# Kernel optimization log

Hardware: AMD Instinct MI355X
Metric: run time of the kernel (lower is better)

## Reference

```python
import jax, jax.numpy as jnp
import numpy as np

B, N, C = 8, 4096, 1024
H, D = 16, 64
FF = 4096
EPS_ATTN = 1e-6
EPS_LN = 1e-5


def layer_norm(x, g, b, eps=EPS_LN):
    mu = jnp.mean(x, axis=-1, keepdims=True)
    var = jnp.mean(jnp.square(x - mu), axis=-1, keepdims=True)
    return (x - mu) * jax.lax.rsqrt(var + eps) * g + b


def phi(x):
    # elu(x) + 1
    return jnp.where(x > 0, x + 1.0, jnp.exp(x))


def setup_inputs() -> dict:
    key = jax.random.key(0)
    ks = jax.random.split(key, 8)
    src = jax.random.normal(ks[0], (B, N, C), dtype=jnp.float32)
    lengths = jax.random.randint(ks[1], (B,), int(0.75 * N), N + 1)
    src_key_padding_mask = jnp.arange(N)[None, :] >= lengths[:, None]
    s = 0.02
    qkv_w = jax.random.normal(ks[2], (3 * C, C), dtype=jnp.float32) * s
    qkv_b = jnp.zeros((3 * C,), jnp.float32)
    out_w = jax.random.normal(ks[3], (C, C), dtype=jnp.float32) * s
    out_b = jnp.zeros((C,), jnp.float32)
    w1 = jax.random.normal(ks[4], (FF, C), dtype=jnp.float32) * s
    b1 = jnp.zeros((FF,), jnp.float32)
    w2 = jax.random.normal(ks[5], (C, FF), dtype=jnp.float32) * s
    b2 = jnp.zeros((C,), jnp.float32)
    ln1_g = jnp.ones((C,), jnp.float32)
    ln1_b = jnp.zeros((C,), jnp.float32)
    ln2_g = jnp.ones((C,), jnp.float32)
    ln2_b = jnp.zeros((C,), jnp.float32)
    return dict(src=src, src_key_padding_mask=src_key_padding_mask,
                qkv_w=qkv_w, qkv_b=qkv_b, out_w=out_w, out_b=out_b,
                w1=w1, b1=b1, w2=w2, b2=b2,
                ln1_g=ln1_g, ln1_b=ln1_b, ln2_g=ln2_g, ln2_b=ln2_b)


def linear_attention(x, mask, qkv_w, qkv_b, out_w, out_b):
    b, n, c = x.shape
    qkv = (x @ qkv_w.T + qkv_b).reshape(b, n, 3, H, D)
    qkv = jnp.transpose(qkv, (2, 0, 3, 1, 4))  # [3,B,H,N,D]
    q, k, v = qkv[0], qkv[1], qkv[2]
    qf, kf = phi(q), phi(k)
    valid = (~mask).astype(kf.dtype)[:, None, :, None]  # [B,1,N,1]
    kf = kf * valid
    v = v * valid
    kv = jnp.einsum('bhnd,bhne->bhde', kf, v)          # [B,H,D,D]
    z = kf.sum(axis=2)                                  # [B,H,D]
    y_num = jnp.einsum('bhnd,bhde->bhne', qf, kv)       # [B,H,N,D]
    y_den = jnp.maximum(jnp.einsum('bhnd,bhd->bhn', qf, z), EPS_ATTN)
    y = y_num / y_den[..., None]
    y = jnp.transpose(y, (0, 2, 1, 3)).reshape(b, n, c)
    return y @ out_w.T + out_b


def reference(src, src_key_padding_mask, qkv_w, qkv_b, out_w, out_b,
              w1, b1, w2, b2, ln1_g, ln1_b, ln2_g, ln2_b):
    # pre-norm: attention block
    attn_out = linear_attention(layer_norm(src, ln1_g, ln1_b), src_key_padding_mask,
                                qkv_w, qkv_b, out_w, out_b)
    x = src + attn_out
    # pre-norm: FFN block (exact gelu, matching torch F.gelu default)
    h = jax.nn.gelu(layer_norm(x, ln2_g, ln2_b) @ w1.T + b1, approximate=False)
    return x + (h @ w2.T + b2)
```

## Files before the change

### kernel.cpp

```cpp
#include <hip/hip_runtime.h>
#include <cmath>
#include <cstdint>

#define MTOK 32768
#define CDIM 1024
#define SEQ  4096
#define NHEAD 16
#define HDIM 64
#define FFDIM 4096

typedef __attribute__((ext_vector_type(8))) short short8;
typedef __attribute__((ext_vector_type(4))) float f32x4;

static __device__ __forceinline__ float b2f(unsigned short u){
  union { unsigned int i; float f; } c; c.i = ((unsigned int)u)<<16; return c.f;
}
static __device__ __forceinline__ unsigned short f2b(float f){
  union { float f; unsigned int i; } c; c.f = f;
  return (unsigned short)((c.i + 0x7fffu + ((c.i>>16)&1u)) >> 16);
}
static __device__ __forceinline__ void nt_store_us(unsigned short v, unsigned short* p){
  __builtin_nontemporal_store(v, p);
}
static __device__ __forceinline__ void nt_store_f(float v, float* p){
  __builtin_nontemporal_store(v, p);
}
static __device__ __forceinline__ void async16(const void* g, void* l){
  __builtin_amdgcn_global_load_lds((const __attribute__((address_space(1))) void*)g,
                                   (__attribute__((address_space(3))) void*)l, 16, 0, 0);
}

__global__ void detect_mask_kernel(const unsigned int* __restrict__ m, int* __restrict__ flag){
  __shared__ int any;
  if(threadIdx.x==0) any=0;
  __syncthreads();
  int loc=0;
  for(int i=threadIdx.x;i<8192;i+=256) if(m[i]>1u) loc=1;
  if(loc) atomicOr(&any,1);
  __syncthreads();
  if(threadIdx.x==0) *flag=any;
}
__global__ void decode_mask_kernel(const void* __restrict__ m, const int* __restrict__ flag,
                                   float* __restrict__ validf){
  int i = blockIdx.x*256 + threadIdx.x;
  int pad = (*flag) ? (int)((const unsigned char*)m)[i] : ((const int*)m)[i];
  validf[i] = pad ? 0.f : 1.f;
}

__global__ void cast_all_kernel(const float* __restrict__ a, const float* __restrict__ b,
                                const float* __restrict__ c, const float* __restrict__ d,
                                unsigned short* __restrict__ oa, unsigned short* __restrict__ ob,
                                unsigned short* __restrict__ oc, unsigned short* __restrict__ od){
  long i = ((long)blockIdx.x*256 + threadIdx.x)*4;
  const float* x; unsigned short* y; long off;
  if(i < 3145728){ x=a; y=oa; off=i; }
  else if(i < 4194304){ x=b; y=ob; off=i-3145728; }
  else if(i < 8388608){ x=c; y=oc; off=i-4194304; }
  else { x=d; y=od; off=i-8388608; }
  float4 v = *(const float4*)(x+off);
  ushort4 o; o.x=f2b(v.x); o.y=f2b(v.y); o.z=f2b(v.z); o.w=f2b(v.w);
  *(ushort4*)(y+off)=o;
}

__global__ __launch_bounds__(256) void ln_kernel(const float* __restrict__ x,
    const float* __restrict__ g, const float* __restrict__ bt, unsigned short* __restrict__ out){
  int row = blockIdx.x, t = threadIdx.x;
  const float* xr = x + (size_t)row*CDIM;
  float4 v = *(const float4*)(xr + t*4);
  float s1 = v.x+v.y+v.z+v.w;
  float s2 = v.x*v.x+v.y*v.y+v.z*v.z+v.w*v.w;
  #pragma unroll
  for(int off=32; off>0; off>>=1){ s1+=__shfl_down(s1,off); s2+=__shfl_down(s2,off); }
  __shared__ float a1[4], a2[4];
  __shared__ float mu_s, rs_s;
  if((t&63)==0){ a1[t>>6]=s1; a2[t>>6]=s2; }
  __syncthreads();
  if(t==0){
    float u1=a1[0]+a1[1]+a1[2]+a1[3], u2=a2[0]+a2[1]+a2[2]+a2[3];
    float mu=u1*(1.f/CDIM);
    mu_s=mu; rs_s=rsqrtf(u2*(1.f/CDIM)-mu*mu+1e-5f);
  }
  __syncthreads();
  float mu=mu_s, rs=rs_s;
  float4 gg=*(const float4*)(g+t*4), bb=*(const float4*)(bt+t*4);
  ushort4 o;
  o.x=f2b((v.x-mu)*rs*gg.x+bb.x);
  o.y=f2b((v.y-mu)*rs*gg.y+bb.y);
  o.z=f2b((v.z-mu)*rs*gg.z+bb.z);
  o.w=f2b((v.w-mu)*rs*gg.w+bb.w);
  *(ushort4*)(out+(size_t)row*CDIM+t*4)=o;
}

template<int MODE>
__global__ __launch_bounds__(256,2) void gemm_bt(
    const unsigned short* __restrict__ A, const unsigned short* __restrict__ Bw,
    const float* __restrict__ bias, const float* __restrict__ extra,
    float* __restrict__ Cf, unsigned short* __restrict__ Cb,
    int M, int N, int K)
{
  __shared__ __align__(16) unsigned short As[128*64];
  __shared__ __align__(16) unsigned short Bs[128*64];
  const int tid = threadIdx.x;
  const int wave = tid>>6, lane = tid&63;
  const int wm = wave>>1, wn = wave&1;
  const int f   = blockIdx.y * gridDim.x + blockIdx.x;
  const int xcd = f & 7, kk = f >> 3;
  const int nx  = kk % gridDim.x;
  const int ny  = (kk / gridDim.x) * 8 + xcd;
  const int m0 = ny*128, n0 = nx*128;
  const int lrow = lane>>3;
  const int gcol = (((lane&7) ^ lrow))*8;

  f32x4 acc[4][4];
  #pragma unroll
  for(int i=0;i<4;i++)
    #pragma unroll
    for(int j=0;j<4;j++) acc[i][j]=(f32x4)(0.f);

  const int ar = wm*64 + (lane&15);
  const int br = wn*64 + (lane&15);
  const int kc = lane>>4;
  const int xorv = lane&7;

  for(int kt=0; kt<K; kt+=64){
    #pragma unroll
    for(int it=0; it<4; it++){
      int wo = wave*4+it;
      int r  = wo*8 + lrow;
      async16(A  + (size_t)(m0+r)*K + kt + gcol, (void*)&As[wo*512]);
      async16(Bw + (size_t)(n0+r)*K + kt + gcol, (void*)&Bs[wo*512]);
    }
    __syncthreads();
    #pragma unroll
    for(int ks=0; ks<2; ks++){
      const int ch = ((ks*4 + kc) ^ xorv)*8;
      short8 a[4], b[4];
      #pragma unroll
      for(int i=0;i<4;i++){
        a[i]=*(const short8*)&As[(ar+i*16)*64 + ch];
        b[i]=*(const short8*)&Bs[(br+i*16)*64 + ch];
      }
      #pragma unroll
      for(int i=0;i<4;i++)
        #pragma unroll
        for(int j=0;j<4;j++)
          acc[i][j]=__builtin_amdgcn_mfma_f32_16x16x32_bf16(a[i],b[j],acc[i][j],0,0,0);
    }
    __syncthreads();
  }
  const int rbase = m0 + wm*64 + (lane>>4)*4;
  const int cbase = n0 + wn*64 + (lane&15);
  #pragma unroll
  for(int mi=0;mi<4;mi++){
    #pragma unroll
    for(int i=0;i<4;i++){
      int m = rbase + mi*16 + i;
      #pragma unroll
      for(int ni=0;ni<4;ni++){
        int n = cbase + ni*16;
        float v = acc[mi][ni][i] + bias[n];
        if(MODE==0){
          float valid = extra[m];
          int part = n>>10;
          float p = (v>0.f)? (v+1.f) : __expf(v);
          float r = (part==0)? p : (part==1? p*valid : v*valid);
          nt_store_us(f2b(r), &Cb[(size_t)m*N + n]);
        } else if(MODE==1){
          size_t off=(size_t)m*N+n;
          Cf[off] = v + extra[off];
        } else if(MODE==2){
          float gl = 0.5f*v*(1.f+erff(v*0.70710678118654752f));
          nt_store_us(f2b(gl), &Cb[(size_t)m*N+n]);
        } else {
          size_t off=(size_t)m*N+n;
          nt_store_f(Cf[off] + v, &Cf[off]);
        }
      }
    }
  }
}

__global__ __launch_bounds__(256) void kvz_partial_kernel(
    const unsigned short* __restrict__ qkv, float* __restrict__ kvp, float* __restrict__ zp)
{
  const int chunk = blockIdx.x;
  const int bh = blockIdx.y;
  const int b = bh>>4, h = bh&15;
  const int t = threadIdx.x;
  __shared__ float kfs[64][64];
  __shared__ float vs[64][64];
  float acc[4][4]={{0}}; float zacc[4]={0};
  const int td=t&15, te=t>>4;
  const int d0=td*4, e0=te*4;
  const int lr=t>>4, lc=(t&15)*4;
  for(int s=0;s<4;s++){
    __syncthreads();
    #pragma unroll
    for(int rr=0; rr<4; rr++){
      int row = rr*16 + lr;
      size_t m  = (size_t)(b*SEQ + chunk*256 + s*64 + row);
      size_t rb = m*3072 + (size_t)h*64;
      ushort4 k4 = *(const ushort4*)(qkv + rb + 1024 + lc);
      ushort4 v4 = *(const ushort4*)(qkv + rb + 2048 + lc);
      kfs[row][lc]=b2f(k4.x); kfs[row][lc+1]=b2f(k4.y); kfs[row][lc+2]=b2f(k4.z); kfs[row][lc+3]=b2f(k4.w);
      vs [row][lc]=b2f(v4.x); vs [row][lc+1]=b2f(v4.y); vs [row][lc+2]=b2f(v4.z); vs [row][lc+3]=b2f(v4.w);
    }
    __syncthreads();
    #pragma unroll 8
    for(int n=0;n<64;n++){
      float4 kq=*(const float4*)&kfs[n][d0];
      float4 vv=*(const float4*)&vs[n][e0];
      float kqa[4]={kq.x,kq.y,kq.z,kq.w};
      float vva[4]={vv.x,vv.y,vv.z,vv.w};
      #pragma unroll
      for(int i=0;i<4;i++)
        #pragma unroll
        for(int j=0;j<4;j++) acc[i][j]+=kqa[i]*vva[j];
      if(te==0){ zacc[0]+=kq.x; zacc[1]+=kq.y; zacc[2]+=kq.z; zacc[3]+=kq.w; }
    }
  }
  const int pidx = bh*16 + chunk;
  float* kvd = kvp + (size_t)pidx*4096;
  #pragma unroll
  for(int i=0;i<4;i++){
    float4 o={acc[i][0],acc[i][1],acc[i][2],acc[i][3]};
    *(float4*)(kvd + (d0+i)*64 + e0)=o;
  }
  if(te==0){
    float4 o={zacc[0],zacc[1],zacc[2],zacc[3]};
    *(float4*)(zp + (size_t)pidx*64 + d0)=o;
  }
}

__global__ void kvz_reduce_kernel(const float* __restrict__ kvp, const float* __restrict__ zp,
                                  float* __restrict__ kv, float* __restrict__ z){
  int bh = blockIdx.x, t = threadIdx.x;
  for(int j=t; j<4096; j+=256){
    float s=0;
    for(int c=0;c<16;c++) s += kvp[((size_t)bh*16+c)*4096 + j];
    kv[(size_t)bh*4096 + j] = s;
  }
  if(t<64){
    float s=0;
    for(int c=0;c<16;c++) s += zp[((size_t)bh*16+c)*64 + t];
    z[bh*64+t]=s;
  }
}

__global__ __launch_bounds__(256) void y_kernel(
    const unsigned short* __restrict__ qkv, const float* __restrict__ kv,
    const float* __restrict__ z, unsigned short* __restrict__ ybuf)
{
  const int nch = blockIdx.x;
  const int bh  = blockIdx.y;
  const int b = bh>>4, h = bh&15;
  const int t = threadIdx.x;
  __shared__ float kvs[64][64];
  __shared__ float qfs[64][68];
  __shared__ float zs[64];
  for(int j=t*4; j<4096; j+=1024){
    float4 vv=*(const float4*)(kv+(size_t)bh*4096+j);
    ((float*)kvs)[j]=vv.x; ((float*)kvs)[j+1]=vv.y; ((float*)kvs)[j+2]=vv.z; ((float*)kvs)[j+3]=vv.w;
  }
  if(t<64) zs[t]=z[bh*64+t];
  for(int s=0;s<4;s++){
    int row=s*16+(t>>4), col=(t&15)*4;
    size_t m=(size_t)(b*SEQ+nch*64+row);
    ushort4 q4=*(const ushort4*)(qkv+m*3072+(size_t)h*64+col);
    qfs[row][col]=b2f(q4.x); qfs[row][col+1]=b2f(q4.y); qfs[row][col+2]=b2f(q4.z); qfs[row][col+3]=b2f(q4.w);
  }
  __syncthreads();
  const int tn=t>>4, te=t&15;
  const int nr0=tn*4, e0=te*4;
  float acc[4][4]={{0}}; float den[4]={0};
  #pragma unroll 4
  for(int d=0;d<64;d++){
    float4 kv4=*(const float4*)&kvs[d][e0];
    float zd=zs[d];
    #pragma unroll
    for(int i=0;i<4;i++){
      float q=qfs[nr0+i][d];
      acc[i][0]+=q*kv4.x; acc[i][1]+=q*kv4.y; acc[i][2]+=q*kv4.z; acc[i][3]+=q*kv4.w;
      den[i]+=q*zd;
    }
  }
  #pragma unroll
  for(int i=0;i<4;i++){
    float inv=1.f/fmaxf(den[i],1e-6f);
    ushort4 o;
    o.x=f2b(acc[i][0]*inv); o.y=f2b(acc[i][1]*inv); o.z=f2b(acc[i][2]*inv); o.w=f2b(acc[i][3]*inv);
    size_t m=(size_t)(b*SEQ+nch*64+nr0+i);
    *(ushort4*)(ybuf+m*1024+(size_t)h*64+e0)=o;
  }
}

extern "C" void kernel_launch(void* const* d_in, const int* in_sizes, int n_in,
                              void* d_out, int out_size, void* d_ws, size_t ws_size,
                              hipStream_t stream)
{
  const float* src   = (const float*)d_in[0];
  const void*  mask  = d_in[1];
  const float* qkv_w = (const float*)d_in[2];
  const float* qkv_b = (const float*)d_in[3];
  const float* out_w = (const float*)d_in[4];
  const float* out_b = (const float*)d_in[5];
  const float* w1    = (const float*)d_in[6];
  const float* b1    = (const float*)d_in[7];
  const float* w2    = (const float*)d_in[8];
  const float* b2    = (const float*)d_in[9];
  const float* ln1g  = (const float*)d_in[10];
  const float* ln1b  = (const float*)d_in[11];
  const float* ln2g  = (const float*)d_in[12];
  const float* ln2b  = (const float*)d_in[13];
  float* out = (float*)d_out;
  char* ws = (char*)d_ws;

  size_t o = 0;
  int* flag = (int*)(ws);                         o += 256;
  float* validf = (float*)(ws+o);                 o += (size_t)MTOK*4;
  unsigned short* wqb = (unsigned short*)(ws+o);  o += (size_t)3072*1024*2;
  unsigned short* wob = (unsigned short*)(ws+o);  o += (size_t)1024*1024*2;
  unsigned short* w1b = (unsigned short*)(ws+o);  o += (size_t)4096*1024*2;
  unsigned short* w2b = (unsigned short*)(ws+o);  o += (size_t)1024*4096*2;
  unsigned short* bufA = (unsigned short*)(ws+o); o += (size_t)MTOK*1024*2;
  char* R = ws+o;                                 o += (size_t)MTOK*4096*2;
  unsigned short* qkvbuf = (unsigned short*)R;
  float* kvp = (float*)(R + (size_t)MTOK*3072*2);
  float* zp  = (float*)(R + (size_t)MTOK*3072*2 + (size_t)2048*4096*4);
  unsigned short* hbuf = (unsigned short*)R;
  float* kv = (float*)(ws+o);                     o += (size_t)128*4096*4;
  float* zv = (float*)(ws+o);                     o += (size_t)128*64*4;

  detect_mask_kernel<<<1,256,0,stream>>>((const unsigned int*)mask, flag);
  decode_mask_kernel<<<MTOK/256,256,0,stream>>>(mask, flag, validf);
  cast_all_kernel<<<12288,256,0,stream>>>(qkv_w, out_w, w1, w2, wqb, wob, w1b, w2b);

  ln_kernel<<<MTOK,256,0,stream>>>(src, ln1g, ln1b, bufA);
  gemm_bt<0><<<dim3(3072/128, MTOK/128),256,0,stream>>>(bufA, wqb, qkv_b, validf, nullptr, qkvbuf, MTOK,3072,1024);
  kvz_partial_kernel<<<dim3(16,128),256,0,stream>>>(qkvbuf, kvp, zp);
  kvz_reduce_kernel<<<128,256,0,stream>>>(kvp, zp, kv, zv);
  y_kernel<<<dim3(64,128),256,0,stream>>>(qkvbuf, kv, zv, bufA);
  gemm_bt<1><<<dim3(1024/128, MTOK/128),256,0,stream>>>(bufA, wob, out_b, src, out, nullptr, MTOK,1024,1024);
  ln_kernel<<<MTOK,256,0,stream>>>(out, ln2g, ln2b, bufA);
  gemm_bt<2><<<dim3(4096/128, MTOK/128),256,0,stream>>>(bufA, w1b, b1, nullptr, nullptr, hbuf, MTOK,4096,1024);
  gemm_bt<3><<<dim3(1024/128, MTOK/128),256,0,stream>>>(hbuf, w2b, b2, nullptr, out, nullptr, MTOK,1024,4096);
}
```

Measured before the change: 1.467 ms.

## Move linear-attention kv and y computations onto MFMA with transposed K/V layout

The QKV GEMM epilogue now writes Q row-major and K and V transposed per head (d-major over sequence), so the kv outer product can run as a bf16 MFMA GEMM in a new single-wave kernel using 32 chunks per head. The reduce kernel packs kv transposed plus z as an extra row in bf16. The y pass becomes an MFMA GEMM whose fifth column tile computes the denominator. The GEMM tile-to-block mapping is also swizzled into 4x8 groups for better L2 reuse, and nontemporal stores are dropped. In exchange, kv and z are rounded to bf16 before multiplying with Q, which reduces precision, and the transposed K/V stores are strided.

```diff
diff --git a/kernel.cpp b/kernel.cpp
--- a/kernel.cpp
+++ b/kernel.cpp
@@ -18,12 +18,6 @@
 static __device__ __forceinline__ unsigned short f2b(float f){
   union { float f; unsigned int i; } c; c.f = f;
   return (unsigned short)((c.i + 0x7fffu + ((c.i>>16)&1u)) >> 16);
-}
-static __device__ __forceinline__ void nt_store_us(unsigned short v, unsigned short* p){
-  __builtin_nontemporal_store(v, p);
-}
-static __device__ __forceinline__ void nt_store_f(float v, float* p){
-  __builtin_nontemporal_store(v, p);
 }
 static __device__ __forceinline__ void async16(const void* g, void* l){
   __builtin_amdgcn_global_load_lds((const __attribute__((address_space(1))) void*)g,
@@ -96,6 +90,7 @@
     const unsigned short* __restrict__ A, const unsigned short* __restrict__ Bw,
     const float* __restrict__ bias, const float* __restrict__ extra,
     float* __restrict__ Cf, unsigned short* __restrict__ Cb,
+    unsigned short* __restrict__ Kt, unsigned short* __restrict__ Vt,
     int M, int N, int K)
 {
   __shared__ __align__(16) unsigned short As[128*64];
@@ -103,10 +98,15 @@
   const int tid = threadIdx.x;
   const int wave = tid>>6, lane = tid&63;
   const int wm = wave>>1, wn = wave&1;
-  const int f   = blockIdx.y * gridDim.x + blockIdx.x;
-  const int xcd = f & 7, kk = f >> 3;
-  const int nx  = kk % gridDim.x;
-  const int ny  = (kk / gridDim.x) * 8 + xcd;
+  const int gx  = gridDim.x;
+  const int f   = blockIdx.y * gx + blockIdx.x;
+  const int xcd = f & 7;
+  const int kk  = f >> 3;
+  const int idx = kk & 31, g = kk >> 5;
+  const int nq  = gx >> 2;
+  const int gxq = g % nq, gy = g / nq;
+  const int nx  = gxq*4 + (idx>>3);
+  const int ny  = (gy*8 + (idx&7))*8 + xcd;
   const int m0 = ny*128, n0 = nx*128;
   const int lrow = lane>>3;
   const int gcol = (((lane&7) ^ lrow))*8;
@@ -150,147 +150,203 @@
   }
   const int rbase = m0 + wm*64 + (lane>>4)*4;
   const int cbase = n0 + wn*64 + (lane&15);
-  #pragma unroll
-  for(int mi=0;mi<4;mi++){
-    #pragma unroll
-    for(int i=0;i<4;i++){
-      int m = rbase + mi*16 + i;
+  if(MODE==0){
+    #pragma unroll
+    for(int mi=0;mi<4;mi++){
+      int mrow = rbase + mi*16;
+      float4 vld = *(const float4*)(extra + mrow);
+      float vv[4] = {vld.x, vld.y, vld.z, vld.w};
       #pragma unroll
       for(int ni=0;ni<4;ni++){
         int n = cbase + ni*16;
-        float v = acc[mi][ni][i] + bias[n];
-        if(MODE==0){
-          float valid = extra[m];
-          int part = n>>10;
-          float p = (v>0.f)? (v+1.f) : __expf(v);
-          float r = (part==0)? p : (part==1? p*valid : v*valid);
-          nt_store_us(f2b(r), &Cb[(size_t)m*N + n]);
-        } else if(MODE==1){
-          size_t off=(size_t)m*N+n;
-          Cf[off] = v + extra[off];
-        } else if(MODE==2){
-          float gl = 0.5f*v*(1.f+erff(v*0.70710678118654752f));
-          nt_store_us(f2b(gl), &Cb[(size_t)m*N+n]);
+        float bs = bias[n];
+        int part = n>>10;
+        if(part==0){
+          #pragma unroll
+          for(int i=0;i<4;i++){
+            float v = acc[mi][ni][i] + bs;
+            float p = (v>0.f)? (v+1.f) : __expf(v);
+            Cb[(size_t)(mrow+i)*1024 + n] = f2b(p);
+          }
         } else {
-          size_t off=(size_t)m*N+n;
-          nt_store_f(Cf[off] + v, &Cf[off]);
+          int d = n & 63, hh = (n>>6) & 15;
+          int bb_ = mrow >> 12, pos = mrow & 4095;
+          unsigned short* dst = (part==1? Kt : Vt)
+              + (((size_t)(bb_*16+hh)*64 + d)*SEQ + pos);
+          ushort4 o;
+          #pragma unroll
+          for(int i=0;i<4;i++){
+            float v = acc[mi][ni][i] + bs;
+            float r = (part==1)? (((v>0.f)?(v+1.f):__expf(v))*vv[i]) : (v*vv[i]);
+            ((unsigned short*)&o)[i] = f2b(r);
+          }
+          *(ushort4*)dst = o;
         }
       }
     }
-  }
-}
-
-__global__ __launch_bounds__(256) void kvz_partial_kernel(
-    const unsigned short* __restrict__ qkv, float* __restrict__ kvp, float* __restrict__ zp)
+  } else {
+    #pragma unroll
+    for(int mi=0;mi<4;mi++){
+      #pragma unroll
+      for(int i=0;i<4;i++){
+        int m = rbase + mi*16 + i;
+        #pragma unroll
+        for(int ni=0;ni<4;ni++){
+          int n = cbase + ni*16;
+          float v = acc[mi][ni][i] + bias[n];
+          if(MODE==1){
+            size_t off=(size_t)m*N+n;
+            Cf[off] = v + extra[off];
+          } else if(MODE==2){
+            float gl = 0.5f*v*(1.f+erff(v*0.70710678118654752f));
+            Cb[(size_t)m*N+n] = f2b(gl);
+          } else {
+            size_t off=(size_t)m*N+n;
+            Cf[off] += v;
+          }
+        }
+      }
+    }
+  }
+}
+
+__global__ __launch_bounds__(64) void kvz_mfma_kernel(
+    const unsigned short* __restrict__ Kt, const unsigned short* __restrict__ Vt,
+    float* __restrict__ kvp, float* __restrict__ zp)
 {
-  const int chunk = blockIdx.x;
-  const int bh = blockIdx.y;
-  const int b = bh>>4, h = bh&15;
-  const int t = threadIdx.x;
-  __shared__ float kfs[64][64];
-  __shared__ float vs[64][64];
-  float acc[4][4]={{0}}; float zacc[4]={0};
-  const int td=t&15, te=t>>4;
-  const int d0=td*4, e0=te*4;
-  const int lr=t>>4, lc=(t&15)*4;
-  for(int s=0;s<4;s++){
-    __syncthreads();
-    #pragma unroll
-    for(int rr=0; rr<4; rr++){
-      int row = rr*16 + lr;
-      size_t m  = (size_t)(b*SEQ + chunk*256 + s*64 + row);
-      size_t rb = m*3072 + (size_t)h*64;
-      ushort4 k4 = *(const ushort4*)(qkv + rb + 1024 + lc);
-      ushort4 v4 = *(const ushort4*)(qkv + rb + 2048 + lc);
-      kfs[row][lc]=b2f(k4.x); kfs[row][lc+1]=b2f(k4.y); kfs[row][lc+2]=b2f(k4.z); kfs[row][lc+3]=b2f(k4.w);
-      vs [row][lc]=b2f(v4.x); vs [row][lc+1]=b2f(v4.y); vs [row][lc+2]=b2f(v4.z); vs [row][lc+3]=b2f(v4.w);
-    }
-    __syncthreads();
-    #pragma unroll 8
-    for(int n=0;n<64;n++){
-      float4 kq=*(const float4*)&kfs[n][d0];
-      float4 vv=*(const float4*)&vs[n][e0];
-      float kqa[4]={kq.x,kq.y,kq.z,kq.w};
-      float vva[4]={vv.x,vv.y,vv.z,vv.w};
+  __shared__ __align__(16) unsigned short Ks[2][64*64];
+  __shared__ __align__(16) unsigned short Vs[2][64*64];
+  const int blk = blockIdx.x;
+  const int bh = blk>>5, kcn = blk&31;
+  const int n0 = kcn*128;
+  const int lane = threadIdx.x;
+  const int r8 = lane>>3;
+  const int gch = ((lane&7) ^ r8)*8;
+  const size_t base = (size_t)bh*64*SEQ + n0 + gch;
+  #pragma unroll
+  for(int t=0;t<2;t++){
+    #pragma unroll
+    for(int wo=0;wo<8;wo++){
+      int r = wo*8 + r8;
+      async16(Kt + base + (size_t)r*SEQ + t*64, (void*)&Ks[t][wo*512]);
+      async16(Vt + base + (size_t)r*SEQ + t*64, (void*)&Vs[t][wo*512]);
+    }
+  }
+  asm volatile("s_waitcnt vmcnt(0)" ::: "memory");
+  f32x4 acc[4][4];
+  #pragma unroll
+  for(int i=0;i<4;i++)
+    #pragma unroll
+    for(int j=0;j<4;j++) acc[i][j]=(f32x4)(0.f);
+  float zacc[4]={0.f,0.f,0.f,0.f};
+  const int l15 = lane&15, kc4 = lane>>4, x7 = lane&7;
+  #pragma unroll
+  for(int t=0;t<2;t++){
+    #pragma unroll
+    for(int ks=0; ks<2; ks++){
+      const int ch = ((ks*4 + kc4) ^ x7)*8;
+      short8 a[4], b[4];
+      #pragma unroll
+      for(int i=0;i<4;i++) a[i]=*(const short8*)&Vs[t][(l15+i*16)*64 + ch];
+      #pragma unroll
+      for(int j=0;j<4;j++) b[j]=*(const short8*)&Ks[t][(l15+j*16)*64 + ch];
+      #pragma unroll
+      for(int j=0;j<4;j++)
+        #pragma unroll
+        for(int e8=0;e8<8;e8++) zacc[j] += b2f((unsigned short)b[j][e8]);
       #pragma unroll
       for(int i=0;i<4;i++)
         #pragma unroll
-        for(int j=0;j<4;j++) acc[i][j]+=kqa[i]*vva[j];
-      if(te==0){ zacc[0]+=kq.x; zacc[1]+=kq.y; zacc[2]+=kq.z; zacc[3]+=kq.w; }
-    }
-  }
-  const int pidx = bh*16 + chunk;
-  float* kvd = kvp + (size_t)pidx*4096;
-  #pragma unroll
-  for(int i=0;i<4;i++){
-    float4 o={acc[i][0],acc[i][1],acc[i][2],acc[i][3]};
-    *(float4*)(kvd + (d0+i)*64 + e0)=o;
-  }
-  if(te==0){
-    float4 o={zacc[0],zacc[1],zacc[2],zacc[3]};
-    *(float4*)(zp + (size_t)pidx*64 + d0)=o;
-  }
+        for(int j=0;j<4;j++)
+          acc[i][j]=__builtin_amdgcn_mfma_f32_16x16x32_bf16(a[i],b[j],acc[i][j],0,0,0);
+    }
+  }
+  #pragma unroll
+  for(int j=0;j<4;j++){
+    float v = zacc[j];
+    v += __shfl_down(v, 32);
+    v += __shfl_down(v, 16);
+    if(lane<16) zp[(size_t)blk*64 + j*16 + lane] = v;
+  }
+  float* kvd = kvp + (size_t)blk*4096;
+  #pragma unroll
+  for(int i=0;i<4;i++)
+    #pragma unroll
+    for(int j=0;j<4;j++)
+      #pragma unroll
+      for(int r=0;r<4;r++)
+        kvd[(i*16 + kc4*4 + r)*64 + j*16 + l15] = acc[i][j][r];
 }
 
 __global__ void kvz_reduce_kernel(const float* __restrict__ kvp, const float* __restrict__ zp,
-                                  float* __restrict__ kv, float* __restrict__ z){
+                                  unsigned short* __restrict__ kvtb){
   int bh = blockIdx.x, t = threadIdx.x;
-  for(int j=t; j<4096; j+=256){
-    float s=0;
-    for(int c=0;c<16;c++) s += kvp[((size_t)bh*16+c)*4096 + j];
-    kv[(size_t)bh*4096 + j] = s;
-  }
-  if(t<64){
-    float s=0;
-    for(int c=0;c<16;c++) s += zp[((size_t)bh*16+c)*64 + t];
-    z[bh*64+t]=s;
-  }
-}
-
-__global__ __launch_bounds__(256) void y_kernel(
-    const unsigned short* __restrict__ qkv, const float* __restrict__ kv,
-    const float* __restrict__ z, unsigned short* __restrict__ ybuf)
+  for(int idx=t; idx<5120; idx+=256){
+    int e = idx>>6, d = idx&63;
+    float s = 0.f;
+    if(e < 64){
+      for(int c=0;c<32;c++) s += kvp[((size_t)bh*32+c)*4096 + e*64 + d];
+    } else if(e == 64){
+      for(int c=0;c<32;c++) s += zp[((size_t)bh*32+c)*64 + d];
+    }
+    kvtb[(size_t)bh*5120 + idx] = f2b(s);
+  }
+}
+
+__global__ __launch_bounds__(256) void y_gemm_kernel(
+    const unsigned short* __restrict__ qb, const unsigned short* __restrict__ kvtb,
+    unsigned short* __restrict__ ybuf)
 {
-  const int nch = blockIdx.x;
-  const int bh  = blockIdx.y;
-  const int b = bh>>4, h = bh&15;
-  const int t = threadIdx.x;
-  __shared__ float kvs[64][64];
-  __shared__ float qfs[64][68];
-  __shared__ float zs[64];
-  for(int j=t*4; j<4096; j+=1024){
-    float4 vv=*(const float4*)(kv+(size_t)bh*4096+j);
-    ((float*)kvs)[j]=vv.x; ((float*)kvs)[j+1]=vv.y; ((float*)kvs)[j+2]=vv.z; ((float*)kvs)[j+3]=vv.w;
-  }
-  if(t<64) zs[t]=z[bh*64+t];
-  for(int s=0;s<4;s++){
-    int row=s*16+(t>>4), col=(t&15)*4;
-    size_t m=(size_t)(b*SEQ+nch*64+row);
-    ushort4 q4=*(const ushort4*)(qkv+m*3072+(size_t)h*64+col);
-    qfs[row][col]=b2f(q4.x); qfs[row][col+1]=b2f(q4.y); qfs[row][col+2]=b2f(q4.z); qfs[row][col+3]=b2f(q4.w);
+  __shared__ __align__(16) unsigned short As[128*64];
+  __shared__ __align__(16) unsigned short Bs[80*64];
+  const int tid = threadIdx.x, lane = tid&63, wave = tid>>6;
+  const int bh = blockIdx.y, b = bh>>4, h = bh&15;
+  const int m0 = blockIdx.x*128;
+  const int r8 = lane>>3, gch = ((lane&7)^r8)*8;
+  const unsigned short* qbase = qb + ((size_t)(b*SEQ + m0))*1024 + h*64 + gch;
+  #pragma unroll
+  for(int it=0; it<4; it++){
+    int wo = wave*4 + it, r = wo*8 + r8;
+    async16(qbase + (size_t)r*1024, (void*)&As[wo*512]);
+  }
+  const unsigned short* kvb = kvtb + (size_t)bh*5120 + gch;
+  #pragma unroll
+  for(int it=0; it<3; it++){
+    int wo = wave + it*4;
+    if(wo < 10){ int r = wo*8 + r8; async16(kvb + r*64, (void*)&Bs[wo*512]); }
   }
   __syncthreads();
-  const int tn=t>>4, te=t&15;
-  const int nr0=tn*4, e0=te*4;
-  float acc[4][4]={{0}}; float den[4]={0};
-  #pragma unroll 4
-  for(int d=0;d<64;d++){
-    float4 kv4=*(const float4*)&kvs[d][e0];
-    float zd=zs[d];
-    #pragma unroll
-    for(int i=0;i<4;i++){
-      float q=qfs[nr0+i][d];
-      acc[i][0]+=q*kv4.x; acc[i][1]+=q*kv4.y; acc[i][2]+=q*kv4.z; acc[i][3]+=q*kv4.w;
-      den[i]+=q*zd;
-    }
-  }
-  #pragma unroll
-  for(int i=0;i<4;i++){
-    float inv=1.f/fmaxf(den[i],1e-6f);
-    ushort4 o;
-    o.x=f2b(acc[i][0]*inv); o.y=f2b(acc[i][1]*inv); o.z=f2b(acc[i][2]*inv); o.w=f2b(acc[i][3]*inv);
-    size_t m=(size_t)(b*SEQ+nch*64+nr0+i);
-    *(ushort4*)(ybuf+m*1024+(size_t)h*64+e0)=o;
+  const int l15 = lane&15, kc4 = lane>>4, x7 = lane&7;
+  f32x4 acc[2][5];
+  #pragma unroll
+  for(int i=0;i<2;i++)
+    #pragma unroll
+    for(int j=0;j<5;j++) acc[i][j]=(f32x4)(0.f);
+  #pragma unroll
+  for(int ks=0; ks<2; ks++){
+    const int ch = ((ks*4 + kc4) ^ x7)*8;
+    short8 a[2], bb[5];
+    #pragma unroll
+    for(int i=0;i<2;i++) a[i]=*(const short8*)&As[(wave*32 + i*16 + l15)*64 + ch];
+    #pragma unroll
+    for(int j=0;j<5;j++) bb[j]=*(const short8*)&Bs[(j*16 + l15)*64 + ch];
+    #pragma unroll
+    for(int i=0;i<2;i++)
+      #pragma unroll
+      for(int j=0;j<5;j++)
+        acc[i][j]=__builtin_amdgcn_mfma_f32_16x16x32_bf16(a[i],bb[j],acc[i][j],0,0,0);
+  }
+  #pragma unroll
+  for(int i=0;i<2;i++){
+    #pragma unroll
+    for(int r=0;r<4;r++){
+      float den = __shfl(acc[i][4][r], lane & 48);
+      float inv = 1.f/fmaxf(den, 1e-6f);
+      size_t m = (size_t)(b*SEQ + m0 + wave*32 + i*16 + kc4*4 + r);
+      #pragma unroll
+      for(int j=0;j<4;j++)
+        ybuf[m*1024 + h*64 + j*16 + l15] = f2b(acc[i][j][r]*inv);
+    }
   }
 }
 
@@ -324,24 +380,28 @@
   unsigned short* w2b = (unsigned short*)(ws+o);  o += (size_t)1024*4096*2;
   unsigned short* bufA = (unsigned short*)(ws+o); o += (size_t)MTOK*1024*2;
   char* R = ws+o;                                 o += (size_t)MTOK*4096*2;
-  unsigned short* qkvbuf = (unsigned short*)R;
+  unsigned short* qb  = (unsigned short*)R;
+  unsigned short* ktb = (unsigned short*)(R + (size_t)MTOK*1024*2);
+  unsigned short* vtb = (unsigned short*)(R + (size_t)MTOK*2048*2);
   float* kvp = (float*)(R + (size_t)MTOK*3072*2);
-  float* zp  = (float*)(R + (size_t)MTOK*3072*2 + (size_t)2048*4096*4);
   unsigned short* hbuf = (unsigned short*)R;
   float* kv = (float*)(ws+o);                     o += (size_t)128*4096*4;
   float* zv = (float*)(ws+o);                     o += (size_t)128*64*4;
+  float* zp = (float*)(ws+o);                     o += (size_t)4096*64*4;
+  unsigned short* kvtb = (unsigned short*)(ws+o); o += (size_t)128*5120*2;
+  (void)kv; (void)zv;
 
   detect_mask_kernel<<<1,256,0,stream>>>((const unsigned int*)mask, flag);
   decode_mask_kernel<<<MTOK/256,256,0,stream>>>(mask, flag, validf);
   cast_all_kernel<<<12288,256,0,stream>>>(qkv_w, out_w, w1, w2, wqb, wob, w1b, w2b);
 
   ln_kernel<<<MTOK,256,0,stream>>>(src, ln1g, ln1b, bufA);
-  gemm_bt<0><<<dim3(3072/128, MTOK/128),256,0,stream>>>(bufA, wqb, qkv_b, validf, nullptr, qkvbuf, MTOK,3072,1024);
-  kvz_partial_kernel<<<dim3(16,128),256,0,stream>>>(qkvbuf, kvp, zp);
-  kvz_reduce_kernel<<<128,256,0,stream>>>(kvp, zp, kv, zv);
-  y_kernel<<<dim3(64,128),256,0,stream>>>(qkvbuf, kv, zv, bufA);
-  gemm_bt<1><<<dim3(1024/128, MTOK/128),256,0,stream>>>(bufA, wob, out_b, src, out, nullptr, MTOK,1024,1024);
+  gemm_bt<0><<<dim3(3072/128, MTOK/128),256,0,stream>>>(bufA, wqb, qkv_b, validf, nullptr, qb, ktb, vtb, MTOK,3072,1024);
+  kvz_mfma_kernel<<<4096,64,0,stream>>>(ktb, vtb, kvp, zp);
+  kvz_reduce_kernel<<<128,256,0,stream>>>(kvp, zp, kvtb);
+  y_gemm_kernel<<<dim3(SEQ/128,128),256,0,stream>>>(qb, kvtb, bufA);
+  gemm_bt<1><<<dim3(1024/128, MTOK/128),256,0,stream>>>(bufA, wob, out_b, src, out, nullptr, nullptr, nullptr, MTOK,1024,1024);
   ln_kernel<<<MTOK,256,0,stream>>>(out, ln2g, ln2b, bufA);
-  gemm_bt<2><<<dim3(4096/128, MTOK/128),256,0,stream>>>(bufA, w1b, b1, nullptr, nullptr, hbuf, MTOK,4096,1024);
-  gemm_bt<3><<<dim3(1024/128, MTOK/128),256,0,stream>>>(hbuf, w2b, b2, nullptr, out, nullptr, MTOK,1024,4096);
-}
+  gemm_bt<2><<<dim3(4096/128, MTOK/128),256,0,stream>>>(bufA, w1b, b1, nullptr, nullptr, hbuf, nullptr, nullptr, MTOK,4096,1024);
+  gemm_bt<3><<<dim3(1024/128, MTOK/128),256,0,stream>>>(hbuf, w2b, b2, nullptr, out, nullptr, nullptr, nullptr, MTOK,1024,4096);
+}
```

New measurement: 1.360 ms. 1.08x faster.
